# Kernel optimization log

Hardware: AMD Instinct MI355X
Metric: run time of the kernel (lower is better)

Reference implementation:

```python
import jax, jax.numpy as jnp
import numpy as np

NUM_HEADS = 12
NUM_GROUPS = 4
METRIC_SCALE = 1.0
CLS_MIX = 1.0
MEAN_MIX = 0.5
ROUTER_SCALE = 1.0
DIFF_SCALE = 1.0
B, N, D, HF = 16, 577, 768, 3072


def _ln(x, g, b, eps=1e-5):
    mu = jnp.mean(x, axis=-1, keepdims=True)
    var = jnp.mean(jnp.square(x - mu), axis=-1, keepdims=True)
    return (x - mu) * jax.lax.rsqrt(var + eps) * g + b


def setup_inputs() -> dict:
    key = jax.random.key(0)
    ks = iter(jax.random.split(key, 16))
    w = lambda shape, std: jax.random.normal(next(ks), shape, jnp.float32) * std
    return {
        "x": w((B, N, D), 1.0),
        "ln1_g": jnp.ones((D,)), "ln1_b": jnp.zeros((D,)),
        "ad_ln_g": jnp.ones((D,)), "ad_ln_b": jnp.zeros((D,)),
        "ad_w": w((D, D), 0.02),
        "w_qkv": w((D, 3 * D), 0.02),
        "w_proj": w((D, D), 0.02), "b_proj": jnp.zeros((D,)),
        "ln2_g": jnp.ones((D,)), "ln2_b": jnp.zeros((D,)),
        "fc1_w": w((D, HF), 0.02), "fc1_b": jnp.zeros((HF,)),
        "fc2_w": w((HF, D), 0.02), "fc2_b": jnp.zeros((D,)),
        "r_ln_g": jnp.ones((HF,)), "r_ln_b": jnp.zeros((HF,)),
        "r_proj_w": w((2 * HF, NUM_GROUPS), 0.02), "r_proj_b": jnp.zeros((NUM_GROUPS,)),
        "r_gate_w": w((2 * HF, 1), 0.02), "r_gate_b": jnp.full((1,), -2.0),
        "r_scale": jnp.full((NUM_GROUPS,), 0.1),
        "d_ln_g": jnp.ones((HF,)), "d_ln_b": jnp.zeros((HF,)),
        "d_out_w": w((HF, HF), 0.005),
        "d_gate_w": w((HF, 1), 0.02), "d_gate_b": jnp.full((1,), -1.5),
    }


def reference(x, ln1_g, ln1_b, ad_ln_g, ad_ln_b, ad_w, w_qkv, w_proj, b_proj,
              ln2_g, ln2_b, fc1_w, fc1_b, fc2_w, fc2_b,
              r_ln_g, r_ln_b, r_proj_w, r_proj_b, r_gate_w, r_gate_b, r_scale,
              d_ln_g, d_ln_b, d_out_w, d_gate_w, d_gate_b):
    b, n, d = x.shape
    hd = d // NUM_HEADS
    # ---- GeoAttention (pre-norm) ----
    h = _ln(x, ln1_g, ln1_b)
    # metric adapter: residual LN+Linear (SharedAttentionMetricAdapter)
    metric_h = h + METRIC_SCALE * (_ln(h, ad_ln_g, ad_ln_b) @ ad_w)
    # q,k from metric path; v from plain path (asymmetric Q/K vs V)
    qk = metric_h @ w_qkv[:, : 2 * d]                # [b,n,2d]
    v = h @ w_qkv[:, 2 * d :]                        # [b,n,d]
    q = qk[..., :d].reshape(b, n, NUM_HEADS, hd).transpose(0, 2, 1, 3)
    k = qk[..., d:].reshape(b, n, NUM_HEADS, hd).transpose(0, 2, 1, 3)
    v = v.reshape(b, n, NUM_HEADS, hd).transpose(0, 2, 1, 3)
    attn = jax.nn.softmax(jnp.einsum("bhnd,bhmd->bhnm", q, k) * (hd ** -0.5), axis=-1)
    out = jnp.einsum("bhnm,bhmd->bhnd", attn, v).transpose(0, 2, 1, 3).reshape(b, n, d)
    x = x + out @ w_proj + b_proj
    # ---- GeoMlp (pre-norm) ----
    h2 = _ln(x, ln2_g, ln2_b)
    hid = h2 @ fc1_w + fc1_b                         # [b,n,HF]
    # GroupCompetitionRouter on hidden
    rn = _ln(hid, r_ln_g, r_ln_b)
    summary = jnp.concatenate([CLS_MIX * rn[:, 0], MEAN_MIX * jnp.mean(rn[:, 1:], axis=1)], axis=-1)  # [b,2HF]
    wts = jax.nn.softmax(summary @ r_proj_w + r_proj_b, axis=-1)       # [b,G]
    gate = jax.nn.sigmoid(summary @ r_gate_w + r_gate_b)               # [b,1]
    centered = wts * float(NUM_GROUPS) - 1.0
    grouped = hid.reshape(b, n, NUM_GROUPS, HF // NUM_GROUPS)
    scale = 1.0 + ROUTER_SCALE * gate[:, None, :, None] * r_scale[None, None, :, None] * centered[:, None, :, None]
    hid = (grouped * scale).reshape(b, n, HF)
    # TokenDiffusionMixer on hidden
    dn = _ln(hid, d_ln_g, d_ln_b)
    tr = dn / jnp.maximum(jnp.linalg.norm(dn, axis=-1, keepdims=True), 1e-12)
    aff = jax.nn.softmax(jnp.einsum("bnc,bmc->bnm", tr, tr) * (HF ** -0.5), axis=-1)
    diffusion = jnp.einsum("bnm,bmc->bnc", aff, dn) - dn
    dgate = jax.nn.sigmoid(dn[:, 0] @ d_gate_w + d_gate_b)             # [b,1]
    hid = hid + DIFF_SCALE * dgate[:, :, None] * (diffusion @ d_out_w)
    # activation + fc2
    hid = jax.nn.gelu(hid, approximate=False)
    return x + hid @ fc2_w + fc2_b
```

## Files before the change

### kernel.cpp

```cpp
#include <hip/hip_runtime.h>
#include <math.h>

typedef unsigned short u16;
typedef unsigned int   u32;
typedef __attribute__((ext_vector_type(4))) float f32x4;
typedef __attribute__((ext_vector_type(4))) u32   u32x4;

#define DEV __device__ __forceinline__

DEV float b2f(u16 u){ u32 x = ((u32)u)<<16; float f; __builtin_memcpy(&f,&x,4); return f; }
DEV u16 f2b(float f){ u32 x; __builtin_memcpy(&x,&f,4); u32 r = x + 0x7FFFu + ((x>>16)&1u); return (u16)(r>>16); }

DEV float ldf(const float* p, long i){ return p[i]; }
DEV float ldf(const u16*   p, long i){ return b2f(p[i]); }

DEV float wave_sum(float v){
#pragma unroll
  for(int o=32;o;o>>=1) v += __shfl_down(v,o,64);
  return v;
}
DEV float wave_max(float v){
#pragma unroll
  for(int o=32;o;o>>=1) v = fmaxf(v, __shfl_down(v,o,64));
  return v;
}
DEV float block_sum(float v, float* tmp){
  v = wave_sum(v);
  if((threadIdx.x&63)==0) tmp[threadIdx.x>>6]=v;
  __syncthreads();
  float r = tmp[0]+tmp[1]+tmp[2]+tmp[3];
  __syncthreads();
  return r;
}
DEV float block_max(float v, float* tmp){
  v = wave_max(v);
  if((threadIdx.x&63)==0) tmp[threadIdx.x>>6]=v;
  __syncthreads();
  float r = fmaxf(fmaxf(tmp[0],tmp[1]),fmaxf(tmp[2],tmp[3]));
  __syncthreads();
  return r;
}

template<typename TI>
__global__ void transpose_pad(const TI* __restrict__ in, u16* __restrict__ out,
                              int R, int C, int Rpad, long strideI, long strideO){
  __shared__ u16 t[32][33];
  in  += (long)blockIdx.z*strideI;
  out += (long)blockIdx.z*strideO;
  int tx = threadIdx.x & 31, ty = threadIdx.x >> 5;
  int bc = blockIdx.x*32, br = blockIdx.y*32;
#pragma unroll
  for(int i=0;i<32;i+=8){
    int r = br+ty+i, c = bc+tx;
    float v = (r<R && c<C) ? ldf(in,(long)r*C+c) : 0.f;
    t[ty+i][tx] = f2b(v);
  }
  __syncthreads();
#pragma unroll
  for(int i=0;i<32;i+=8){
    int c = bc+ty+i, r = br+tx;
    if(c<C && r<Rpad) out[(long)c*Rpad + r] = t[tx][ty+i];
  }
}

template<typename TI>
__global__ void ln_rows(const TI* __restrict__ x, const float* __restrict__ g,
                        const float* __restrict__ b, u16* __restrict__ y, int W){
  __shared__ float tmp[4];
  long base=(long)blockIdx.x*W;
  float s=0.f, ss=0.f;
  for(int c=threadIdx.x;c<W;c+=256){ float v=ldf(x,base+c); s+=v; ss+=v*v; }
  s=block_sum(s,tmp); ss=block_sum(ss,tmp);
  float mu=s/W;
  float rstd=rsqrtf(fmaxf(ss/W-mu*mu,0.f)+1e-5f);
  for(int c=threadIdx.x;c<W;c+=256){
    float v=ldf(x,base+c);
    y[base+c]=f2b((v-mu)*rstd*g[c]+b[c]);
  }
}

__global__ void row_stats(const u16* __restrict__ x, float* __restrict__ stats, int W){
  __shared__ float tmp[4];
  long base=(long)blockIdx.x*W;
  float s=0.f,ss=0.f;
  for(int c=threadIdx.x;c<W;c+=256){ float v=b2f(x[base+c]); s+=v; ss+=v*v; }
  s=block_sum(s,tmp); ss=block_sum(ss,tmp);
  if(threadIdx.x==0){
    float mu=s/W;
    stats[2*(long)blockIdx.x]=mu;
    stats[2*(long)blockIdx.x+1]=rsqrtf(fmaxf(ss/W-mu*mu,0.f)+1e-5f);
  }
}

__global__ void dn_kernel(const u16* __restrict__ x, const float* __restrict__ g,
                          const float* __restrict__ b, u16* __restrict__ dn,
                          float* __restrict__ rn){
  const int W=3072;
  __shared__ float tmp[4];
  long base=(long)blockIdx.x*(long)W;
  float s=0.f,ss=0.f;
  for(int c=threadIdx.x;c<W;c+=256){ float v=b2f(x[base+c]); s+=v; ss+=v*v; }
  s=block_sum(s,tmp); ss=block_sum(ss,tmp);
  float mu=s/W;
  float rstd=rsqrtf(fmaxf(ss/W-mu*mu,0.f)+1e-5f);
  float sq=0.f;
  for(int c=threadIdx.x;c<W;c+=256){
    float v=(b2f(x[base+c])-mu)*rstd*g[c]+b[c];
    sq+=v*v;
  }
  sq=block_sum(sq,tmp);
  float r=1.f/fmaxf(sqrtf(sq),1e-12f);
  for(int c=threadIdx.x;c<W;c+=256){
    float v=(b2f(x[base+c])-mu)*rstd*g[c]+b[c];
    dn[base+c]=f2b(v);
  }
  if(threadIdx.x==0) rn[blockIdx.x]=r;
}

__global__ void softmax_rows(u16* __restrict__ S, int W, int Wp,
                             const float* __restrict__ rs, int rpb, float alpha){
  __shared__ float tmp[4];
  long row = blockIdx.x;
  u16* p = S + row*(long)Wp;
  float rowscale = alpha;
  const float* rsb = nullptr;
  if(rs){ long bt=row/rpb; int m=(int)(row%rpb); rsb = rs + bt*(long)rpb; rowscale *= rsb[m]; }
  float mx=-3e38f;
  for(int c=threadIdx.x;c<W;c+=256){
    float v=b2f(p[c])*rowscale; if(rs) v*=rsb[c];
    mx=fmaxf(mx,v);
  }
  mx=block_max(mx,tmp);
  float sm=0.f;
  for(int c=threadIdx.x;c<W;c+=256){
    float v=b2f(p[c])*rowscale; if(rs) v*=rsb[c];
    sm+=__expf(v-mx);
  }
  sm=block_sum(sm,tmp);
  float inv=1.f/sm;
  for(int c=threadIdx.x;c<W;c+=256){
    float v=b2f(p[c])*rowscale; if(rs) v*=rsb[c];
    p[c]=f2b(__expf(v-mx)*inv);
  }
  for(int c=W+threadIdx.x;c<Wp;c+=256) p[c]=0;
}

__global__ void split_heads(const u16* __restrict__ qk, u16* __restrict__ qh, u16* __restrict__ kh){
  int i = blockIdx.x*256+threadIdx.x;
  if(i >= 16*577*12*8) return;
  int dv = i&7; int h=(i>>3)%12; int bn=i/96;
  int b=bn/577, n=bn%577;
  long src=(long)bn*1536 + h*64 + dv*8;
  long dst=((long)((b*12+h)*577+n))*64 + dv*8;
  *(u32x4*)(qh+dst) = *(const u32x4*)(qk+src);
  *(u32x4*)(kh+dst) = *(const u32x4*)(qk+src+768);
}
__global__ void merge_heads(const u16* __restrict__ aoh, u16* __restrict__ aout){
  int i = blockIdx.x*256+threadIdx.x;
  if(i >= 16*577*12*8) return;
  int dv=i&7; int h=(i>>3)%12; int bn=i/96;
  int b=bn/577, n=bn%577;
  long dst=(long)bn*768 + h*64 + dv*8;
  long src=((long)((b*12+h)*577+n))*64 + dv*8;
  *(u32x4*)(aout+dst) = *(const u32x4*)(aoh+src);
}
__global__ void make_vT(const u16* __restrict__ v, u16* __restrict__ vT){
  long i = (long)blockIdx.x*256+threadIdx.x;
  if(i >= (long)192*64*608) return;
  int n=(int)(i%608); long q=i/608; int d=(int)(q&63); int bh=(int)(q>>6);
  int b=bh/12, h=bh%12;
  u16 val=0;
  if(n<577) val = v[((long)(b*577+n))*768 + h*64 + d];
  vT[i]=val;
}

__global__ void summary_kernel(const u16* __restrict__ hid, const float* __restrict__ stats,
                               const float* __restrict__ rg, const float* __restrict__ rb,
                               float* __restrict__ summ){
  int b=blockIdx.y;
  int c=blockIdx.x*256+threadIdx.x;
  const u16* hb=hid+(size_t)b*577*3072;
  const float* st=stats+(size_t)b*577*2;
  float g=rg[c], be=rb[c];
  float cls=(b2f(hb[c])-st[0])*st[1]*g+be;
  float acc=0.f;
  for(int n=1;n<577;n++) acc += (b2f(hb[(size_t)n*3072+c])-st[2*n])*st[2*n+1];
  summ[(size_t)b*6144+c]        = 1.0f*cls;
  summ[(size_t)b*6144+3072+c]   = 0.5f*(g*(acc*(1.f/576.f))+be);
}

__global__ void router_kernel(const float* __restrict__ summ, const float* __restrict__ pw,
                              const float* __restrict__ pb, const float* __restrict__ gw,
                              const float* __restrict__ gb, const float* __restrict__ rsc,
                              float* __restrict__ scalef){
  __shared__ float tmp[4];
  int b=blockIdx.x;
  float a0=0,a1=0,a2=0,a3=0,a4=0;
  for(int c=threadIdx.x;c<6144;c+=256){
    float sv=summ[(size_t)b*6144+c];
    a0+=sv*pw[c*4+0]; a1+=sv*pw[c*4+1]; a2+=sv*pw[c*4+2]; a3+=sv*pw[c*4+3];
    a4+=sv*gw[c];
  }
  a0=block_sum(a0,tmp); a1=block_sum(a1,tmp); a2=block_sum(a2,tmp);
  a3=block_sum(a3,tmp); a4=block_sum(a4,tmp);
  if(threadIdx.x==0){
    float l0=a0+pb[0], l1=a1+pb[1], l2=a2+pb[2], l3=a3+pb[3];
    float mx=fmaxf(fmaxf(l0,l1),fmaxf(l2,l3));
    float e0=__expf(l0-mx),e1=__expf(l1-mx),e2=__expf(l2-mx),e3=__expf(l3-mx);
    float s=e0+e1+e2+e3;
    float gate=1.f/(1.f+__expf(-(a4+gb[0])));
    float w0=e0/s,w1=e1/s,w2=e2/s,w3=e3/s;
    scalef[b*4+0]=1.f+gate*rsc[0]*(4.f*w0-1.f);
    scalef[b*4+1]=1.f+gate*rsc[1]*(4.f*w1-1.f);
    scalef[b*4+2]=1.f+gate*rsc[2]*(4.f*w2-1.f);
    scalef[b*4+3]=1.f+gate*rsc[3]*(4.f*w3-1.f);
  }
}

__global__ void scale_hid(u16* __restrict__ hid, const float* __restrict__ scalef){
  long i=(long)blockIdx.x*256+threadIdx.x;
  if(i >= (long)9232*3072/8) return;
  long e=i*8;
  int c=(int)(e%3072);
  int b=(int)((e/3072)/577);
  float sc=scalef[b*4 + c/768];
  u32x4 u = *(u32x4*)(hid+e);
  u16* pu=(u16*)&u;
#pragma unroll
  for(int j=0;j<8;j++) pu[j]=f2b(b2f(pu[j])*sc);
  *(u32x4*)(hid+e)=u;
}

__global__ void dgate_kernel(const u16* __restrict__ dn, const float* __restrict__ gw,
                             const float* __restrict__ gb, float* __restrict__ dgate){
  __shared__ float tmp[4];
  int b=blockIdx.x;
  const u16* row = dn + (size_t)b*577*3072;
  float a=0.f;
  for(int c=threadIdx.x;c<3072;c+=256) a+=b2f(row[c])*gw[c];
  a=block_sum(a,tmp);
  if(threadIdx.x==0) dgate[b]=1.f/(1.f+__expf(-(a+gb[0])));
}

constexpr int F_BIAS=1, F_RES=2, F_GELU=4, F_GATE=8, F_RESF32=16, F_OUTF32=32;

DEV int swz(int u){ int row=u>>2, sl=u&3; return row*4 + (sl ^ ((row>>1)&3)); }

template<int FLAGS>
__global__ __launch_bounds__(256,2) void gemm_bt(
  const u16* __restrict__ A, long lda, long szA,
  const u16* __restrict__ B, long ldb, long szB,
  void* __restrict__ Cv, long ldc, long szC,
  const float* __restrict__ bias,
  const void* __restrict__ resv, long ldr, long szR, float res_scale,
  const float* __restrict__ gate,
  float alpha, int M, int N, int K)
{
  __shared__ u16 shA[128*32];
  __shared__ u16 shB[128*32];
  const int z = blockIdx.z;
  A += (long)z*szA; B += (long)z*szB;
  const int tid=threadIdx.x, lane=tid&63, wid=tid>>6;
  const int wr=wid>>1, wc=wid&1;
  const long m0=(long)blockIdx.x*128, n0=(long)blockIdx.y*128;
  f32x4 acc[4][4];
#pragma unroll
  for(int i=0;i<4;i++)
#pragma unroll
    for(int j=0;j<4;j++){ f32x4 zv={0.f,0.f,0.f,0.f}; acc[i][j]=zv; }

  const int u0=tid, u1=256+tid;
  const int r0_=u0>>2, kc0=(u0&3)*8;
  const int r1_=u1>>2, kc1=(u1&3)*8;
  for(int k0=0;k0<K;k0+=32){
    long ar0 = m0 + r0_; if(ar0>=M) ar0=M-1;
    long ar1 = m0 + r1_; if(ar1>=M) ar1=M-1;
    long br0 = n0 + r0_; if(br0>=N) br0=N-1;
    long br1 = n0 + r1_; if(br1>=N) br1=N-1;
    u32x4 ra0 = *(const u32x4*)(A + ar0*lda + k0 + kc0);
    u32x4 ra1 = *(const u32x4*)(A + ar1*lda + k0 + kc1);
    u32x4 rb0 = *(const u32x4*)(B + br0*ldb + k0 + kc0);
    u32x4 rb1 = *(const u32x4*)(B + br1*ldb + k0 + kc1);
    __syncthreads();
    ((u32x4*)shA)[swz(u0)] = ra0;
    ((u32x4*)shA)[swz(u1)] = ra1;
    ((u32x4*)shB)[swz(u0)] = rb0;
    ((u32x4*)shB)[swz(u1)] = rb1;
    __syncthreads();
    const int ks = lane>>4, rr = lane&15;
    u32x4 av[4], bv[4];
#pragma unroll
    for(int mi=0;mi<4;mi++) av[mi] = ((const u32x4*)shA)[swz((wr*64+mi*16+rr)*4+ks)];
#pragma unroll
    for(int ni=0;ni<4;ni++) bv[ni] = ((const u32x4*)shB)[swz((wc*64+ni*16+rr)*4+ks)];
#pragma unroll
    for(int mi=0;mi<4;mi++)
#pragma unroll
      for(int ni=0;ni<4;ni++)
        asm volatile("v_mfma_f32_16x16x32_bf16 %0, %1, %2, %0"
                     : "+v"(acc[mi][ni]) : "v"(av[mi]), "v"(bv[ni]));
  }
  const float* resf = (const float*)resv + (long)z*szR;
  const u16*   resh = (const u16*)resv   + (long)z*szR;
  float* Cf = (float*)Cv + (long)z*szC;
  u16*   Ch = (u16*)Cv   + (long)z*szC;
  float gv = (FLAGS&F_GATE)? gate[z] : 1.f;
#pragma unroll
  for(int mi=0;mi<4;mi++){
#pragma unroll
    for(int ni=0;ni<4;ni++){
      long c0 = n0 + wc*64 + ni*16 + (lane&15);
      if(c0>=N) continue;
      float bb = (FLAGS&F_BIAS)? bias[c0] : 0.f;
#pragma unroll
      for(int r=0;r<4;r++){
        long rw = m0 + wr*64 + mi*16 + (lane>>4)*4 + r;
        if(rw>=M) continue;
        float t = acc[mi][ni][r]*alpha*gv + bb;
        if(FLAGS&F_RES){
          float rvv = (FLAGS&F_RESF32)? resf[rw*ldr+c0] : b2f(resh[rw*ldr+c0]);
          t += res_scale*rvv;
        }
        if(FLAGS&F_GELU) t = 0.5f*t*(1.f+erff(t*0.70710678118654752f));
        if(FLAGS&F_OUTF32) Cf[rw*ldc+c0]=t;
        else               Ch[rw*ldc+c0]=f2b(t);
      }
    }
  }
}

static inline dim3 ggrid(int M,int N,int nb){ return dim3((M+127)/128,(N+127)/128,nb); }

extern "C" void kernel_launch(void* const* d_in, const int* in_sizes, int n_in,
                              void* d_out, int out_size, void* d_ws, size_t ws_size,
                              hipStream_t stream){
  const int BNr=16*577;
  const float* x      = (const float*)d_in[0];
  const float* ln1_g  = (const float*)d_in[1];
  const float* ln1_b  = (const float*)d_in[2];
  const float* ad_ln_g= (const float*)d_in[3];
  const float* ad_ln_b= (const float*)d_in[4];
  const float* ad_w   = (const float*)d_in[5];
  const float* w_qkv  = (const float*)d_in[6];
  const float* w_proj = (const float*)d_in[7];
  const float* b_proj = (const float*)d_in[8];
  const float* ln2_g  = (const float*)d_in[9];
  const float* ln2_b  = (const float*)d_in[10];
  const float* fc1_w  = (const float*)d_in[11];
  const float* fc1_b  = (const float*)d_in[12];
  const float* fc2_w  = (const float*)d_in[13];
  const float* fc2_b  = (const float*)d_in[14];
  const float* r_ln_g = (const float*)d_in[15];
  const float* r_ln_b = (const float*)d_in[16];
  const float* r_proj_w=(const float*)d_in[17];
  const float* r_proj_b=(const float*)d_in[18];
  const float* r_gate_w=(const float*)d_in[19];
  const float* r_gate_b=(const float*)d_in[20];
  const float* r_scale =(const float*)d_in[21];
  const float* d_ln_g = (const float*)d_in[22];
  const float* d_ln_b = (const float*)d_in[23];
  const float* d_outw = (const float*)d_in[24];
  const float* d_gate_w=(const float*)d_in[25];
  const float* d_gate_b=(const float*)d_in[26];

  char* ws=(char*)d_ws;
  size_t off=0;
  auto take=[&](size_t nb){ size_t r=off; off=(off+nb+255)&~(size_t)255; return r; };
  auto al  =[&](size_t v){ return (v+255)&~(size_t)255; };
  const size_t o_qkvT = take((size_t)2304*768*2);
  const size_t o_adT  = take((size_t)768*768*2);
  const size_t o_projT= take((size_t)768*768*2);
  const size_t o_fc1T = take((size_t)3072*768*2);
  const size_t o_fc2T = take((size_t)768*3072*2);
  const size_t o_doutT= take((size_t)3072*3072*2);
  const size_t o_x2   = take((size_t)BNr*768*4);
  const size_t o_hid  = take((size_t)BNr*3072*2);
  const size_t o_stats= take((size_t)BNr*2*4);
  const size_t o_rn   = take((size_t)BNr*4);
  const size_t o_sum  = take((size_t)16*6144*4);
  const size_t o_scalef=take(64*4);
  const size_t o_dg   = take(64);
  const size_t o_h    = take((size_t)BNr*768*2);
  const size_t o_lnh  = take((size_t)BNr*768*2);
  const size_t o_metric=take((size_t)BNr*768*2);
  const size_t o_qk   = take((size_t)BNr*1536*2);
  const size_t o_v    = take((size_t)BNr*768*2);
  const size_t o_qh   = take((size_t)192*577*64*2);
  const size_t o_kh   = take((size_t)192*577*64*2);
  const size_t o_vT   = take((size_t)192*64*608*2);
  (void)o_v; (void)o_vT; (void)ws_size; (void)in_sizes; (void)n_in; (void)out_size;
  const size_t o_S    = o_qk;
  const size_t o_aoh  = o_metric;
  const size_t o_aout = o_h;
  const size_t o_h2   = o_lnh;
  const size_t o_dn   = o_h;
  const size_t o_aff  = al(o_dn + (size_t)BNr*3072*2);
  const size_t o_dnTb = al(o_aff + (size_t)16*577*608*2);
  const size_t o_diff = al(o_dnTb + (size_t)4*3072*608*2);
  const size_t o_hact = o_dn;

  u16* qkvT=(u16*)(ws+o_qkvT); u16* adT=(u16*)(ws+o_adT); u16* projT=(u16*)(ws+o_projT);
  u16* fc1T=(u16*)(ws+o_fc1T); u16* fc2T=(u16*)(ws+o_fc2T); u16* doutT=(u16*)(ws+o_doutT);
  float* x2=(float*)(ws+o_x2); u16* hid=(u16*)(ws+o_hid);
  float* stats=(float*)(ws+o_stats); float* rn=(float*)(ws+o_rn);
  float* summ=(float*)(ws+o_sum); float* scalef=(float*)(ws+o_scalef); float* dgate=(float*)(ws+o_dg);
  u16* hbuf=(u16*)(ws+o_h); u16* lnh=(u16*)(ws+o_lnh); u16* metric=(u16*)(ws+o_metric);
  u16* qkbuf=(u16*)(ws+o_qk); u16* vbuf=(u16*)(ws+o_v);
  u16* qh=(u16*)(ws+o_qh); u16* kh=(u16*)(ws+o_kh); u16* vT=(u16*)(ws+o_vT);
  u16* Sc=(u16*)(ws+o_S); u16* aoh=(u16*)(ws+o_aoh); u16* aout=(u16*)(ws+o_aout);
  u16* h2=(u16*)(ws+o_h2);
  u16* dn=(u16*)(ws+o_dn); u16* aff=(u16*)(ws+o_aff); u16* dnTb=(u16*)(ws+o_dnTb);
  u16* diff=(u16*)(ws+o_diff); u16* hact=(u16*)(ws+o_hact);

  dim3 blk(256);
  transpose_pad<float><<<dim3(72,24,1),blk,0,stream>>>(w_qkv, qkvT, 768,2304,768, 0,0);
  transpose_pad<float><<<dim3(24,24,1),blk,0,stream>>>(ad_w,  adT,  768,768, 768, 0,0);
  transpose_pad<float><<<dim3(24,24,1),blk,0,stream>>>(w_proj,projT,768,768, 768, 0,0);
  transpose_pad<float><<<dim3(96,24,1),blk,0,stream>>>(fc1_w, fc1T, 768,3072,768, 0,0);
  transpose_pad<float><<<dim3(24,96,1),blk,0,stream>>>(fc2_w, fc2T, 3072,768,3072,0,0);
  transpose_pad<float><<<dim3(96,96,1),blk,0,stream>>>(d_outw,doutT,3072,3072,3072,0,0);
  ln_rows<float><<<BNr,blk,0,stream>>>(x, ln1_g, ln1_b, hbuf, 768);
  ln_rows<u16>  <<<BNr,blk,0,stream>>>(hbuf, ad_ln_g, ad_ln_b, lnh, 768);
  gemm_bt<F_RES><<<ggrid(BNr,768,1),blk,0,stream>>>(lnh,768,0, adT,768,0, metric,768,0,
      nullptr, hbuf,768,0, 1.f, nullptr, 1.f, BNr,768,768);
  gemm_bt<0><<<ggrid(BNr,1536,1),blk,0,stream>>>(metric,768,0, qkvT,768,0, qkbuf,1536,0,
      nullptr, nullptr,0,0,0.f, nullptr, 1.f, BNr,1536,768);
  gemm_bt<0><<<ggrid(BNr,768,1),blk,0,stream>>>(hbuf,768,0, qkvT+(size_t)1536*768,768,0, vbuf,768,0,
      nullptr, nullptr,0,0,0.f, nullptr, 1.f, BNr,768,768);
  split_heads<<<3462,blk,0,stream>>>(qkbuf, qh, kh);
  make_vT<<<29184,blk,0,stream>>>(vbuf, vT);
  for(int c=0;c<6;c++){
    const u16* qc=qh+(size_t)c*32*577*64;
    const u16* kc=kh+(size_t)c*32*577*64;
    gemm_bt<0><<<dim3(5,5,32),blk,0,stream>>>(qc,64,(long)577*64, kc,64,(long)577*64,
        Sc,608,(long)577*608, nullptr, nullptr,0,0,0.f, nullptr, 0.125f, 577,577,64);
    softmax_rows<<<32*577,blk,0,stream>>>(Sc,577,608, nullptr,577, 1.f);
    gemm_bt<0><<<dim3(5,1,32),blk,0,stream>>>(Sc,608,(long)577*608, vT+(size_t)c*32*64*608,608,(long)64*608,
        aoh+(size_t)c*32*577*64,64,(long)577*64, nullptr, nullptr,0,0,0.f, nullptr, 1.f, 577,64,608);
  }
  merge_heads<<<3462,blk,0,stream>>>(aoh, aout);
  gemm_bt<F_RES|F_BIAS|F_RESF32|F_OUTF32><<<ggrid(BNr,768,1),blk,0,stream>>>(aout,768,0, projT,768,0,
      x2,768,0, b_proj, x,768,0, 1.f, nullptr, 1.f, BNr,768,768);
  ln_rows<float><<<BNr,blk,0,stream>>>(x2, ln2_g, ln2_b, h2, 768);
  gemm_bt<F_BIAS><<<ggrid(BNr,3072,1),blk,0,stream>>>(h2,768,0, fc1T,768,0, hid,3072,0,
      fc1_b, nullptr,0,0,0.f, nullptr, 1.f, BNr,3072,768);
  row_stats<<<BNr,blk,0,stream>>>(hid, stats, 3072);
  summary_kernel<<<dim3(12,16),blk,0,stream>>>(hid, stats, r_ln_g, r_ln_b, summ);
  router_kernel<<<16,blk,0,stream>>>(summ, r_proj_w, r_proj_b, r_gate_w, r_gate_b, r_scale, scalef);
  scale_hid<<<13848,blk,0,stream>>>(hid, scalef);
  dn_kernel<<<BNr,blk,0,stream>>>(hid, d_ln_g, d_ln_b, dn, rn);
  dgate_kernel<<<16,blk,0,stream>>>(dn, d_gate_w, d_gate_b, dgate);
  gemm_bt<0><<<dim3(5,5,16),blk,0,stream>>>(dn,3072,(long)577*3072, dn,3072,(long)577*3072,
      aff,608,(long)577*608, nullptr, nullptr,0,0,0.f, nullptr, 1.f, 577,577,3072);
  softmax_rows<<<BNr,blk,0,stream>>>(aff,577,608, rn,577, 0.01804219634f);
  for(int g4=0; g4<4; ++g4){
    transpose_pad<u16><<<dim3(96,19,4),blk,0,stream>>>(dn+(size_t)g4*4*577*3072, dnTb,
        577,3072,608, (long)577*3072, (long)3072*608);
    gemm_bt<F_RES><<<dim3(5,24,4),blk,0,stream>>>(aff+(size_t)g4*4*577*608,608,(long)577*608,
        dnTb,608,(long)3072*608, diff+(size_t)g4*4*577*3072,3072,(long)577*3072,
        nullptr, dn+(size_t)g4*4*577*3072,3072,(long)577*3072, -1.f, nullptr, 1.f, 577,3072,608);
  }
  gemm_bt<F_RES|F_GATE|F_GELU><<<dim3(5,24,16),blk,0,stream>>>(diff,3072,(long)577*3072,
      doutT,3072,0, hact,3072,(long)577*3072, nullptr, hid,3072,(long)577*3072, 1.f,
      dgate, 1.f, 577,3072,3072);
  gemm_bt<F_RES|F_BIAS|F_RESF32|F_OUTF32><<<ggrid(BNr,768,1),blk,0,stream>>>(hact,3072,0,
      fc2T,3072,0, d_out,768,0, fc2_b, x2,768,0, 1.f, nullptr, 1.f, BNr,768,3072);
}
```

Measured before the change: 1.668 ms.

## Load GEMM tiles directly into LDS and remap workgroups across XCDs

The bf16 GEMM now uses global_load_lds to copy A/B tiles straight into shared memory, with the swizzle applied on the global side. This removes the register staging and the separate LDS store instructions. The grid is flattened to 1D and block ids are remapped so that consecutive tiles land on the same XCD, which should improve L2 reuse. The risks are that loads still are not double-buffered, so latency is exposed between barriers, and that correctness of the direct-to-LDS path depends on the per-wave layout matching the swizzle.

Result: faster. 1.553 ms (-6.9%).

```diff
diff --git a/kernel.cpp b/kernel.cpp
--- a/kernel.cpp
+++ b/kernel.cpp
@@ -7,12 +7,19 @@
 typedef __attribute__((ext_vector_type(4))) u32   u32x4;
 
 #define DEV __device__ __forceinline__
+#define AS1 __attribute__((address_space(1)))
+#define AS3 __attribute__((address_space(3)))
 
 DEV float b2f(u16 u){ u32 x = ((u32)u)<<16; float f; __builtin_memcpy(&f,&x,4); return f; }
 DEV u16 f2b(float f){ u32 x; __builtin_memcpy(&x,&f,4); u32 r = x + 0x7FFFu + ((x>>16)&1u); return (u16)(r>>16); }
 
 DEV float ldf(const float* p, long i){ return p[i]; }
 DEV float ldf(const u16*   p, long i){ return b2f(p[i]); }
+
+DEV void gload16(const u16* g, u16* l){
+  __builtin_amdgcn_global_load_lds((const AS1 u32*)(const void*)g,
+                                   (AS3 u32*)(void*)l, 16, 0, 0);
+}
 
 DEV float wave_sum(float v){
 #pragma unroll
@@ -254,38 +261,49 @@
   const float* __restrict__ bias,
   const void* __restrict__ resv, long ldr, long szR, float res_scale,
   const float* __restrict__ gate,
-  float alpha, int M, int N, int K)
+  float alpha, int M, int N, int K, int NX, int NY)
 {
-  __shared__ u16 shA[128*32];
-  __shared__ u16 shB[128*32];
-  const int z = blockIdx.z;
+  __shared__ alignas(16) u16 shA[128*32];
+  __shared__ alignas(16) u16 shB[128*32];
+  const int nwg = (int)gridDim.x;
+  const int orig = (int)blockIdx.x;
+  const int q = nwg>>3, r = nwg&7;
+  const int xcd = orig&7, idx = orig>>3;
+  const int wg = (xcd<r ? xcd*(q+1) : r*(q+1)+(xcd-r)*q) + idx;
+  const int bx = wg % NX; const int t_ = wg / NX;
+  const int by = t_ % NY; const int z  = t_ / NY;
+
   A += (long)z*szA; B += (long)z*szB;
   const int tid=threadIdx.x, lane=tid&63, wid=tid>>6;
   const int wr=wid>>1, wc=wid&1;
-  const long m0=(long)blockIdx.x*128, n0=(long)blockIdx.y*128;
+  const long m0=(long)bx*128, n0=(long)by*128;
   f32x4 acc[4][4];
 #pragma unroll
   for(int i=0;i<4;i++)
 #pragma unroll
     for(int j=0;j<4;j++){ f32x4 zv={0.f,0.f,0.f,0.f}; acc[i][j]=zv; }
 
-  const int u0=tid, u1=256+tid;
-  const int r0_=u0>>2, kc0=(u0&3)*8;
-  const int r1_=u1>>2, kc1=(u1&3)*8;
+  const int lr = lane>>2, lsl = lane&3;
+  const u16* pA[2]; const u16* pB[2]; u16* lA[2]; u16* lB[2];
+#pragma unroll
+  for(int i=0;i<2;i++){
+    int ra = wid*32 + i*16 + lr;
+    int kc = (lsl ^ ((ra>>1)&3))*8;
+    long gr = m0+ra; if(gr>=M) gr=M-1;
+    long gb = n0+ra; if(gb>=N) gb=N-1;
+    pA[i] = A + gr*lda + kc;
+    pB[i] = B + gb*ldb + kc;
+    lA[i] = shA + (wid*32 + i*16)*32;
+    lB[i] = shB + (wid*32 + i*16)*32;
+  }
+
   for(int k0=0;k0<K;k0+=32){
-    long ar0 = m0 + r0_; if(ar0>=M) ar0=M-1;
-    long ar1 = m0 + r1_; if(ar1>=M) ar1=M-1;
-    long br0 = n0 + r0_; if(br0>=N) br0=N-1;
-    long br1 = n0 + r1_; if(br1>=N) br1=N-1;
-    u32x4 ra0 = *(const u32x4*)(A + ar0*lda + k0 + kc0);
-    u32x4 ra1 = *(const u32x4*)(A + ar1*lda + k0 + kc1);
-    u32x4 rb0 = *(const u32x4*)(B + br0*ldb + k0 + kc0);
-    u32x4 rb1 = *(const u32x4*)(B + br1*ldb + k0 + kc1);
     __syncthreads();
-    ((u32x4*)shA)[swz(u0)] = ra0;
-    ((u32x4*)shA)[swz(u1)] = ra1;
-    ((u32x4*)shB)[swz(u0)] = rb0;
-    ((u32x4*)shB)[swz(u1)] = rb1;
+#pragma unroll
+    for(int i=0;i<2;i++){
+      gload16(pA[i]+k0, lA[i]);
+      gload16(pB[i]+k0, lB[i]);
+    }
     __syncthreads();
     const int ks = lane>>4, rr = lane&15;
     u32x4 av[4], bv[4];
@@ -313,10 +331,10 @@
       if(c0>=N) continue;
       float bb = (FLAGS&F_BIAS)? bias[c0] : 0.f;
 #pragma unroll
-      for(int r=0;r<4;r++){
-        long rw = m0 + wr*64 + mi*16 + (lane>>4)*4 + r;
+      for(int r2=0;r2<4;r2++){
+        long rw = m0 + wr*64 + mi*16 + (lane>>4)*4 + r2;
         if(rw>=M) continue;
-        float t = acc[mi][ni][r]*alpha*gv + bb;
+        float t = acc[mi][ni][r2]*alpha*gv + bb;
         if(FLAGS&F_RES){
           float rvv = (FLAGS&F_RESF32)? resf[rw*ldr+c0] : b2f(resh[rw*ldr+c0]);
           t += res_scale*rvv;
@@ -329,7 +347,9 @@
   }
 }
 
-static inline dim3 ggrid(int M,int N,int nb){ return dim3((M+127)/128,(N+127)/128,nb); }
+static inline int gpack(int M,int N,int nb,int& NX,int& NY){
+  NX=(M+127)/128; NY=(N+127)/128; return NX*NY*nb;
+}
 
 extern "C" void kernel_launch(void* const* d_in, const int* in_sizes, int n_in,
                               void* d_out, int out_size, void* d_ws, size_t ws_size,
@@ -413,6 +433,7 @@
   u16* diff=(u16*)(ws+o_diff); u16* hact=(u16*)(ws+o_hact);
 
   dim3 blk(256);
+  int NX, NY, ng;
   transpose_pad<float><<<dim3(72,24,1),blk,0,stream>>>(w_qkv, qkvT, 768,2304,768, 0,0);
   transpose_pad<float><<<dim3(24,24,1),blk,0,stream>>>(ad_w,  adT,  768,768, 768, 0,0);
   transpose_pad<float><<<dim3(24,24,1),blk,0,stream>>>(w_proj,projT,768,768, 768, 0,0);
@@ -421,48 +442,59 @@
   transpose_pad<float><<<dim3(96,96,1),blk,0,stream>>>(d_outw,doutT,3072,3072,3072,0,0);
   ln_rows<float><<<BNr,blk,0,stream>>>(x, ln1_g, ln1_b, hbuf, 768);
   ln_rows<u16>  <<<BNr,blk,0,stream>>>(hbuf, ad_ln_g, ad_ln_b, lnh, 768);
-  gemm_bt<F_RES><<<ggrid(BNr,768,1),blk,0,stream>>>(lnh,768,0, adT,768,0, metric,768,0,
-      nullptr, hbuf,768,0, 1.f, nullptr, 1.f, BNr,768,768);
-  gemm_bt<0><<<ggrid(BNr,1536,1),blk,0,stream>>>(metric,768,0, qkvT,768,0, qkbuf,1536,0,
-      nullptr, nullptr,0,0,0.f, nullptr, 1.f, BNr,1536,768);
-  gemm_bt<0><<<ggrid(BNr,768,1),blk,0,stream>>>(hbuf,768,0, qkvT+(size_t)1536*768,768,0, vbuf,768,0,
-      nullptr, nullptr,0,0,0.f, nullptr, 1.f, BNr,768,768);
+  ng=gpack(BNr,768,1,NX,NY);
+  gemm_bt<F_RES><<<ng,blk,0,stream>>>(lnh,768,0, adT,768,0, metric,768,0,
+      nullptr, hbuf,768,0, 1.f, nullptr, 1.f, BNr,768,768, NX,NY);
+  ng=gpack(BNr,1536,1,NX,NY);
+  gemm_bt<0><<<ng,blk,0,stream>>>(metric,768,0, qkvT,768,0, qkbuf,1536,0,
+      nullptr, nullptr,0,0,0.f, nullptr, 1.f, BNr,1536,768, NX,NY);
+  ng=gpack(BNr,768,1,NX,NY);
+  gemm_bt<0><<<ng,blk,0,stream>>>(hbuf,768,0, qkvT+(size_t)1536*768,768,0, vbuf,768,0,
+      nullptr, nullptr,0,0,0.f, nullptr, 1.f, BNr,768,768, NX,NY);
   split_heads<<<3462,blk,0,stream>>>(qkbuf, qh, kh);
   make_vT<<<29184,blk,0,stream>>>(vbuf, vT);
   for(int c=0;c<6;c++){
     const u16* qc=qh+(size_t)c*32*577*64;
     const u16* kc=kh+(size_t)c*32*577*64;
-    gemm_bt<0><<<dim3(5,5,32),blk,0,stream>>>(qc,64,(long)577*64, kc,64,(long)577*64,
-        Sc,608,(long)577*608, nullptr, nullptr,0,0,0.f, nullptr, 0.125f, 577,577,64);
+    ng=gpack(577,577,32,NX,NY);
+    gemm_bt<0><<<ng,blk,0,stream>>>(qc,64,(long)577*64, kc,64,(long)577*64,
+        Sc,608,(long)577*608, nullptr, nullptr,0,0,0.f, nullptr, 0.125f, 577,577,64, NX,NY);
     softmax_rows<<<32*577,blk,0,stream>>>(Sc,577,608, nullptr,577, 1.f);
-    gemm_bt<0><<<dim3(5,1,32),blk,0,stream>>>(Sc,608,(long)577*608, vT+(size_t)c*32*64*608,608,(long)64*608,
-        aoh+(size_t)c*32*577*64,64,(long)577*64, nullptr, nullptr,0,0,0.f, nullptr, 1.f, 577,64,608);
+    ng=gpack(577,64,32,NX,NY);
+    gemm_bt<0><<<ng,blk,0,stream>>>(Sc,608,(long)577*608, vT+(size_t)c*32*64*608,608,(long)64*608,
+        aoh+(size_t)c*32*577*64,64,(long)577*64, nullptr, nullptr,0,0,0.f, nullptr, 1.f, 577,64,608, NX,NY);
   }
   merge_heads<<<3462,blk,0,stream>>>(aoh, aout);
-  gemm_bt<F_RES|F_BIAS|F_RESF32|F_OUTF32><<<ggrid(BNr,768,1),blk,0,stream>>>(aout,768,0, projT,768,0,
-      x2,768,0, b_proj, x,768,0, 1.f, nullptr, 1.f, BNr,768,768);
+  ng=gpack(BNr,768,1,NX,NY);
+  gemm_bt<F_RES|F_BIAS|F_RESF32|F_OUTF32><<<ng,blk,0,stream>>>(aout,768,0, projT,768,0,
+      x2,768,0, b_proj, x,768,0, 1.f, nullptr, 1.f, BNr,768,768, NX,NY);
   ln_rows<float><<<BNr,blk,0,stream>>>(x2, ln2_g, ln2_b, h2, 768);
-  gemm_bt<F_BIAS><<<ggrid(BNr,3072,1),blk,0,stream>>>(h2,768,0, fc1T,768,0, hid,3072,0,
-      fc1_b, nullptr,0,0,0.f, nullptr, 1.f, BNr,3072,768);
+  ng=gpack(BNr,3072,1,NX,NY);
+  gemm_bt<F_BIAS><<<ng,blk,0,stream>>>(h2,768,0, fc1T,768,0, hid,3072,0,
+      fc1_b, nullptr,0,0,0.f, nullptr, 1.f, BNr,3072,768, NX,NY);
   row_stats<<<BNr,blk,0,stream>>>(hid, stats, 3072);
   summary_kernel<<<dim3(12,16),blk,0,stream>>>(hid, stats, r_ln_g, r_ln_b, summ);
   router_kernel<<<16,blk,0,stream>>>(summ, r_proj_w, r_proj_b, r_gate_w, r_gate_b, r_scale, scalef);
   scale_hid<<<13848,blk,0,stream>>>(hid, scalef);
   dn_kernel<<<BNr,blk,0,stream>>>(hid, d_ln_g, d_ln_b, dn, rn);
   dgate_kernel<<<16,blk,0,stream>>>(dn, d_gate_w, d_gate_b, dgate);
-  gemm_bt<0><<<dim3(5,5,16),blk,0,stream>>>(dn,3072,(long)577*3072, dn,3072,(long)577*3072,
-      aff,608,(long)577*608, nullptr, nullptr,0,0,0.f, nullptr, 1.f, 577,577,3072);
+  ng=gpack(577,577,16,NX,NY);
+  gemm_bt<0><<<ng,blk,0,stream>>>(dn,3072,(long)577*3072, dn,3072,(long)577*3072,
+      aff,608,(long)577*608, nullptr, nullptr,0,0,0.f, nullptr, 1.f, 577,577,3072, NX,NY);
   softmax_rows<<<BNr,blk,0,stream>>>(aff,577,608, rn,577, 0.01804219634f);
   for(int g4=0; g4<4; ++g4){
     transpose_pad<u16><<<dim3(96,19,4),blk,0,stream>>>(dn+(size_t)g4*4*577*3072, dnTb,
         577,3072,608, (long)577*3072, (long)3072*608);
-    gemm_bt<F_RES><<<dim3(5,24,4),blk,0,stream>>>(aff+(size_t)g4*4*577*608,608,(long)577*608,
+    ng=gpack(577,3072,4,NX,NY);
+    gemm_bt<F_RES><<<ng,blk,0,stream>>>(aff+(size_t)g4*4*577*608,608,(long)577*608,
         dnTb,608,(long)3072*608, diff+(size_t)g4*4*577*3072,3072,(long)577*3072,
-        nullptr, dn+(size_t)g4*4*577*3072,3072,(long)577*3072, -1.f, nullptr, 1.f, 577,3072,608);
-  }
-  gemm_bt<F_RES|F_GATE|F_GELU><<<dim3(5,24,16),blk,0,stream>>>(diff,3072,(long)577*3072,
+        nullptr, dn+(size_t)g4*4*577*3072,3072,(long)577*3072, -1.f, nullptr, 1.f, 577,3072,608, NX,NY);
+  }
+  ng=gpack(577,3072,16,NX,NY);
+  gemm_bt<F_RES|F_GATE|F_GELU><<<ng,blk,0,stream>>>(diff,3072,(long)577*3072,
       doutT,3072,0, hact,3072,(long)577*3072, nullptr, hid,3072,(long)577*3072, 1.f,
-      dgate, 1.f, 577,3072,3072);
-  gemm_bt<F_RES|F_BIAS|F_RESF32|F_OUTF32><<<ggrid(BNr,768,1),blk,0,stream>>>(hact,3072,0,
-      fc2T,3072,0, d_out,768,0, fc2_b, x2,768,0, 1.f, nullptr, 1.f, BNr,768,3072);
-}
+      dgate, 1.f, 577,3072,3072, NX,NY);
+  ng=gpack(BNr,768,1,NX,NY);
+  gemm_bt<F_RES|F_BIAS|F_RESF32|F_OUTF32><<<ng,blk,0,stream>>>(hact,3072,0,
+      fc2T,3072,0, d_out,768,0, fc2_b, x2,768,0, 1.f, nullptr, 1.f, BNr,768,3072, NX,NY);
+}
```
